# Kernel optimization log

Hardware: AMD Instinct MI355X
Metric: run time of the kernel (lower is better)

The kernel has to match this reference:

```python
import jax, jax.numpy as jnp
import numpy as np

N_NODES = 50000
N_EDGES = 800000
IN_CH = 128
OUT_CH = 64


def setup_inputs() -> dict:
    key = jax.random.key(0)
    ks = jax.random.split(key, 8)
    cat = IN_CH + OUT_CH
    scale = 1.0 / np.sqrt(cat)
    return {
        "x": jax.random.normal(ks[0], (N_NODES, IN_CH), dtype=jnp.float32),
        "edge_index": jax.random.randint(ks[1], (2, N_EDGES), 0, N_NODES, dtype=jnp.int64),
        "edge_weight": jax.random.uniform(ks[2], (N_EDGES,), dtype=jnp.float32),
        "hidden_state": jax.random.normal(ks[3], (N_NODES, OUT_CH), dtype=jnp.float32),
        "W_z": jax.random.normal(ks[4], (cat, OUT_CH), dtype=jnp.float32) * scale,
        "b_z": jnp.zeros((OUT_CH,), dtype=jnp.float32),
        "W_r": jax.random.normal(ks[5], (cat, OUT_CH), dtype=jnp.float32) * scale,
        "b_r": jnp.zeros((OUT_CH,), dtype=jnp.float32),
        "W_h": jax.random.normal(ks[6], (cat, OUT_CH), dtype=jnp.float32) * scale,
        "b_h": jnp.zeros((OUT_CH,), dtype=jnp.float32),
    }


def _gcn_norm(row, col, w, num_nodes):
    # PyG GCNConv normalization with self-loops (fill_value=1):
    # norm_e = deg[row]^-1/2 * w_e * deg[col]^-1/2 over loop-augmented edges
    loops = jnp.arange(num_nodes, dtype=row.dtype)
    row = jnp.concatenate([row, loops])
    col = jnp.concatenate([col, loops])
    w = jnp.concatenate([w, jnp.ones((num_nodes,), dtype=w.dtype)])
    deg = jax.ops.segment_sum(w, col, num_segments=num_nodes)
    dinv = jnp.where(deg > 0, jax.lax.rsqrt(deg), 0.0)
    norm = dinv[row] * w * dinv[col]
    return row, col, norm


def _gcn_conv(x_cat, W, b, row, col, norm, num_nodes):
    h = x_cat @ W                                   # (N, out)
    msg = h[row] * norm[:, None]                    # (E+N, out) gather + scale
    out = jax.ops.segment_sum(msg, col, num_segments=num_nodes)
    return out + b


def reference(x, edge_index, edge_weight, hidden_state,
              W_z, b_z, W_r, b_r, W_h, b_h):
    n = x.shape[0]
    row, col, norm = _gcn_norm(edge_index[0], edge_index[1], edge_weight, n)
    xh = jnp.concatenate([x, hidden_state], axis=1)
    z = jax.nn.sigmoid(_gcn_conv(xh, W_z, b_z, row, col, norm, n))
    r = jax.nn.sigmoid(_gcn_conv(xh, W_r, b_r, row, col, norm, n))
    xrh = jnp.concatenate([x, r * hidden_state], axis=1)
    h_cand = jnp.tanh(_gcn_conv(xrh, W_h, b_h, row, col, norm, n))
    return z * hidden_state + (1.0 - z) * h_cand
```

## Files before the change

### kernel.cpp

```cpp
#include <hip/hip_runtime.h>
#include <hip/hip_bf16.h>
#include <cstdint>
#include <cstddef>

#define IN_CH   128
#define OUT_CH  64
#define CAT_CH  192

typedef short bf16x8 __attribute__((ext_vector_type(8)));
typedef float f32x4  __attribute__((ext_vector_type(4)));
typedef float f32x2  __attribute__((ext_vector_type(2)));
typedef unsigned long long u64;
typedef unsigned int u32;

__device__ __forceinline__ float sigmoidf_(float x) { return 1.f / (1.f + __expf(-x)); }

__device__ __forceinline__ unsigned short f2bf(float f) {
    u32 u = __float_as_uint(f);
    u32 r = (u + 0x7fffu + ((u >> 16) & 1u)) >> 16;
    return (unsigned short)r;
}
__device__ __forceinline__ float bflo(u32 v) { return __uint_as_float(v << 16); }
__device__ __forceinline__ float bfhi(u32 v) { return __uint_as_float(v & 0xffff0000u); }

__device__ __forceinline__ unsigned char f2e4m3(float f) {
    u32 p = __builtin_amdgcn_cvt_pk_fp8_f32(f, f, 0, false);
    return (unsigned char)p;
}
template <bool HI>
__device__ __forceinline__ f32x2 fp8pk(u32 v) {
    return __builtin_amdgcn_cvt_pk_f32_fp8((int)v, HI);
}

__global__ void detect_kernel(const unsigned int* __restrict__ ei, int* __restrict__ flag) {
    unsigned int v = ei[(threadIdx.x << 1) + 1];
    unsigned long long b = __ballot(v != 0u);
    if (threadIdx.x == 0) *flag = (b != 0ull) ? 1 : 0;
}

__device__ __forceinline__ int load_col(const void* ei, int i, int E, int f) {
    return f ? ((const int*)ei)[E + i] : (int)((const long long*)ei)[E + i];
}
__device__ __forceinline__ int load_row(const void* ei, int i, int E, int f) {
    return f ? ((const int*)ei)[i] : (int)((const long long*)ei)[i];
}

__global__ void zero16_kernel(int4* __restrict__ p, int n16) {
    int i = blockIdx.x * blockDim.x + threadIdx.x;
    if (i < n16) p[i] = make_int4(0, 0, 0, 0);
}

__global__ void hist2_kernel(const void* __restrict__ ei, const float* __restrict__ w,
                             u64* __restrict__ packed8, u32* __restrict__ rank,
                             const int* __restrict__ flag, int E, int N) {
    int i0 = (blockIdx.x * blockDim.x + threadIdx.x) * 2;
    if (i0 >= E) return;
    const u32 shard = blockIdx.x & 7;
    u64* __restrict__ shp = packed8 + (size_t)shard * N;
    int f = *flag;
    u32 rk[2];
#pragma unroll
    for (int k = 0; k < 2; k++) {
        int i = i0 + k;
        if (i < E) {
            int c = load_col(ei, i, E, f);
            u32 wq = __float2uint_rn(w[i] * 1048576.0f);
            u64 old = atomicAdd(&shp[c], (1ull << 32) | (u64)wq);
            rk[k] = (shard << 28) | (u32)(old >> 32);
        }
    }
#pragma unroll
    for (int k = 0; k < 2; k++)
        if (i0 + k < E) rank[i0 + k] = rk[k];
}

__global__ __launch_bounds__(256) void scan1_kernel(const u64* __restrict__ packed8,
                                                    float* __restrict__ dinv,
                                                    u32* __restrict__ shoff,
                                                    int* __restrict__ starts,
                                                    int* __restrict__ bsum, int n) {
    __shared__ int s[256];
    int i = blockIdx.x * 256 + threadIdx.x;
    int v = 0;
    if (i < n) {
        u32 run = 0, wsum = 0;
#pragma unroll
        for (int sh = 0; sh < 8; sh++) {
            u64 p = packed8[(size_t)sh * n + i];
            shoff[(size_t)sh * n + i] = run;
            run  += (u32)(p >> 32);
            wsum += (u32)p;
        }
        float ws = (float)wsum * (1.0f / 1048576.0f);
        dinv[i] = rsqrtf(1.0f + ws);
        v = (int)run;
    }
    s[threadIdx.x] = v;
    __syncthreads();
#pragma unroll
    for (int d = 1; d < 256; d <<= 1) {
        int t = (threadIdx.x >= d) ? s[threadIdx.x - d] : 0;
        __syncthreads();
        s[threadIdx.x] += t;
        __syncthreads();
    }
    if (i < n) starts[i] = s[threadIdx.x] - v;
    if (threadIdx.x == 255) bsum[blockIdx.x] = s[255];
}

__global__ __launch_bounds__(256) void scan2_kernel(int* __restrict__ bsum, int nb) {
    __shared__ int s[256];
    int t = threadIdx.x;
    int v = (t < nb) ? bsum[t] : 0;
    s[t] = v;
    __syncthreads();
#pragma unroll
    for (int d = 1; d < 256; d <<= 1) {
        int u = (t >= d) ? s[t - d] : 0;
        __syncthreads();
        s[t] += u;
        __syncthreads();
    }
    if (t < nb) bsum[t] = s[t] - v;
}

__global__ void scan3_kernel(int* __restrict__ starts, const int* __restrict__ boff,
                             int n, int E) {
    int i = blockIdx.x * blockDim.x + threadIdx.x;
    if (i == 0) starts[n] = E;
    if (i < n) starts[i] += boff[blockIdx.x];
}

__global__ void scatter2_kernel(const void* __restrict__ ei, const float* __restrict__ w,
                                const float* __restrict__ dinv, const int* __restrict__ starts,
                                const u32* __restrict__ shoff, const u32* __restrict__ rank,
                                u64* __restrict__ pairs, const int* __restrict__ flag,
                                int E, int N) {
    int i0 = (blockIdx.x * blockDim.x + threadIdx.x) * 4;
    if (i0 >= E) return;
    int f = *flag;
    int r[4], c[4];
#pragma unroll
    for (int k = 0; k < 4; k++) {
        int i = i0 + k;
        if (i < E) { r[k] = load_row(ei, i, E, f); c[k] = load_col(ei, i, E, f); }
    }
#pragma unroll
    for (int k = 0; k < 4; k++) {
        int i = i0 + k;
        if (i < E) {
            float nm = dinv[r[k]] * w[i] * dinv[c[k]];
            u32 rk = rank[i];
            u32 sh = rk >> 28, rks = rk & 0x0fffffffu;
            int pos = starts[c[k]] + (int)shoff[(size_t)sh * N + c[k]] + (int)rks;
            pairs[pos] = ((u64)__float_as_uint(nm) << 32) | (u32)(r[k] << 7);
        }
    }
}

__global__ void cvt_kernel(const float* __restrict__ x, const float* __restrict__ hidden,
                           unsigned short* __restrict__ xb, unsigned short* __restrict__ hb,
                           int nx, int nh) {
    int i4 = (blockIdx.x * blockDim.x + threadIdx.x) * 4;
    if (i4 < nx) {
        float4 v = *(const float4*)&x[i4];
        ushort4 o = { f2bf(v.x), f2bf(v.y), f2bf(v.z), f2bf(v.w) };
        *(ushort4*)&xb[i4] = o;
    } else {
        int j = i4 - nx;
        if (j < nh) {
            float4 v = *(const float4*)&hidden[j];
            ushort4 o = { f2bf(v.x), f2bf(v.y), f2bf(v.z), f2bf(v.w) };
            *(ushort4*)&hb[j] = o;
        }
    }
}

__global__ void packW_kernel(const float* __restrict__ Wz, const float* __restrict__ Wr,
                             const float* __restrict__ Wh,
                             unsigned short* __restrict__ Bzrt, unsigned short* __restrict__ Wht) {
    int i = blockIdx.x * blockDim.x + threadIdx.x;
    if (i >= 192 * CAT_CH) return;
    int col = i / CAT_CH, k = i % CAT_CH;
    if (col < 128) {
        float v = (col < 64) ? Wz[k * 64 + col] : Wr[k * 64 + (col - 64)];
        Bzrt[col * CAT_CH + k] = f2bf(v);
    } else {
        Wht[(col - 128) * CAT_CH + k] = f2bf(Wh[k * 64 + (col - 128)]);
    }
}

template <int TN, bool FP8OUT>
__global__ __launch_bounds__(256) void gemm_bf16_kernel(
    const unsigned short* __restrict__ A0, int a0w,
    const unsigned short* __restrict__ A1, int a1w,
    const unsigned short* __restrict__ Bt,
    void* __restrict__ Cout, int nrows)
{
    __shared__ unsigned short As[128][48];
    __shared__ unsigned short Bs[TN][200];

    const int t = threadIdx.x, lane = t & 63, wave = t >> 6;
    const int rowBase = blockIdx.x * 128;

    for (int idx = t * 8; idx < TN * CAT_CH; idx += 256 * 8) {
        int col = idx / CAT_CH, k = idx % CAT_CH;
        *(int4*)&Bs[col][k] = *(const int4*)&Bt[idx];
    }

    f32x4 acc[2][TN / 16];
#pragma unroll
    for (int rf = 0; rf < 2; rf++)
#pragma unroll
        for (int cf = 0; cf < TN / 16; cf++) acc[rf][cf] = (f32x4){0.f, 0.f, 0.f, 0.f};

    const int srow = t >> 1, half = t & 1;
    int arow = rowBase + srow;
    if (arow >= nrows) arow = nrows - 1;

    for (int k0 = 0; k0 < CAT_CH; k0 += 32) {
        __syncthreads();
        {
            const unsigned short* src = (k0 < a0w)
                ? A0 + (size_t)arow * a0w + k0
                : A1 + (size_t)arow * a1w + (k0 - a0w);
            *(int4*)&As[srow][half * 16] = *(const int4*)(src + half * 16);
            *(int4*)&As[srow][half * 16 + 8] = *(const int4*)(src + half * 16 + 8);
        }
        __syncthreads();

        const int rbase = wave * 32;
        const int koff = (lane >> 4) * 8;
        bf16x8 a0 = *(const bf16x8*)&As[rbase + (lane & 15)][koff];
        bf16x8 a1 = *(const bf16x8*)&As[rbase + 16 + (lane & 15)][koff];
#pragma unroll
        for (int cf = 0; cf < TN / 16; cf++) {
            bf16x8 b = *(const bf16x8*)&Bs[cf * 16 + (lane & 15)][k0 + koff];
            acc[0][cf] = __builtin_amdgcn_mfma_f32_16x16x32_bf16(a0, b, acc[0][cf], 0, 0, 0);
            acc[1][cf] = __builtin_amdgcn_mfma_f32_16x16x32_bf16(a1, b, acc[1][cf], 0, 0, 0);
        }
    }

#pragma unroll
    for (int rf = 0; rf < 2; rf++)
#pragma unroll
        for (int cf = 0; cf < TN / 16; cf++) {
            int row0 = rowBase + wave * 32 + rf * 16 + (lane >> 4) * 4;
            int col  = cf * 16 + (lane & 15);
#pragma unroll
            for (int r = 0; r < 4; r++) {
                int row = row0 + r;
                if (row < nrows) {
                    if (FP8OUT)
                        ((unsigned char*)Cout)[(size_t)row * TN + col] = f2e4m3(acc[rf][cf][r]);
                    else
                        ((unsigned short*)Cout)[(size_t)row * TN + col] = f2bf(acc[rf][cf][r]);
                }
            }
        }
}

__global__ __launch_bounds__(256) void spmm_zr_kernel(
    const unsigned char* __restrict__ H8, const u64* __restrict__ pairs,
    const int* __restrict__ starts, const float* __restrict__ dinv,
    const float* __restrict__ hidden, const float* __restrict__ bz,
    const float* __restrict__ br, float* __restrict__ Z,
    unsigned short* __restrict__ RHb, int N)
{
    int node = (blockIdx.x * 256 + threadIdx.x) >> 6;
    if (node >= N) return;
    const int lane = threadIdx.x & 63;
    const int sub = lane & 31, half = lane >> 5;
    int s = starts[node], e = starts[node + 1];
    float d = dinv[node], d2 = d * d;

    float a0 = 0.f, a1 = 0.f, a2 = 0.f, a3 = 0.f;
    if (half == 0) {
        u32 sv = *(const u32*)&H8[(size_t)node * 128 + sub * 4];
        f32x2 s01 = fp8pk<false>(sv), s23 = fp8pk<true>(sv);
        a0 = s01.x * d2; a1 = s01.y * d2; a2 = s23.x * d2; a3 = s23.y * d2;
    }

    int j = s;
    int full = s + ((e - s) & ~15);
    for (; j < full; j += 16) {
        u32 hv[8]; float nm[8];
#pragma unroll
        for (int k = 0; k < 8; k++) {
            u64 p = pairs[j + k * 2 + half];
            nm[k] = __uint_as_float((u32)(p >> 32));
            hv[k] = *(const u32*)&H8[(size_t)(u32)p + sub * 4];
        }
#pragma unroll
        for (int k = 0; k < 8; k++) {
            f32x2 h01 = fp8pk<false>(hv[k]), h23 = fp8pk<true>(hv[k]);
            a0 = fmaf(h01.x, nm[k], a0); a1 = fmaf(h01.y, nm[k], a1);
            a2 = fmaf(h23.x, nm[k], a2); a3 = fmaf(h23.y, nm[k], a3);
        }
    }
    if (j < e) {
        u32 hv[8]; float nm[8];
#pragma unroll
        for (int k = 0; k < 8; k++) {
            int jj = j + k * 2 + half;
            u64 p = pairs[(jj < e) ? jj : (e - 1)];
            nm[k] = (jj < e) ? __uint_as_float((u32)(p >> 32)) : 0.f;
            hv[k] = *(const u32*)&H8[(size_t)(u32)p + sub * 4];
        }
#pragma unroll
        for (int k = 0; k < 8; k++) {
            f32x2 h01 = fp8pk<false>(hv[k]), h23 = fp8pk<true>(hv[k]);
            a0 = fmaf(h01.x, nm[k], a0); a1 = fmaf(h01.y, nm[k], a1);
            a2 = fmaf(h23.x, nm[k], a2); a3 = fmaf(h23.y, nm[k], a3);
        }
    }

    a0 += __shfl_xor(a0, 32, 64);
    a1 += __shfl_xor(a1, 32, 64);
    a2 += __shfl_xor(a2, 32, 64);
    a3 += __shfl_xor(a3, 32, 64);

    if (half == 0) {
        if (sub < 16) {
            int c = sub * 4;
            float4 b4 = *(const float4*)&bz[c];
            float4 o = { sigmoidf_(a0 + b4.x), sigmoidf_(a1 + b4.y),
                         sigmoidf_(a2 + b4.z), sigmoidf_(a3 + b4.w) };
            *(float4*)&Z[(size_t)node * 64 + c] = o;
        } else {
            int c = (sub - 16) * 4;
            float4 b4 = *(const float4*)&br[c];
            float4 hid = *(const float4*)&hidden[(size_t)node * 64 + c];
            float r0 = sigmoidf_(a0 + b4.x) * hid.x;
            float r1 = sigmoidf_(a1 + b4.y) * hid.y;
            float r2 = sigmoidf_(a2 + b4.z) * hid.z;
            float r3 = sigmoidf_(a3 + b4.w) * hid.w;
            ushort4 o = { f2bf(r0), f2bf(r1), f2bf(r2), f2bf(r3) };
            *(ushort4*)&RHb[(size_t)node * 64 + c] = o;
        }
    }
}

__global__ __launch_bounds__(256) void spmm_h_kernel(
    const unsigned short* __restrict__ H, const u64* __restrict__ pairs,
    const int* __restrict__ starts, const float* __restrict__ dinv,
    const float* __restrict__ hidden, const float* __restrict__ bh,
    const float* __restrict__ Z, float* __restrict__ out, int N)
{
    int node = (blockIdx.x * 256 + threadIdx.x) >> 6;
    if (node >= N) return;
    const int lane = threadIdx.x & 63;
    const int sub = lane & 31, half = lane >> 5;
    const unsigned char* Hb = (const unsigned char*)H;
    int s = starts[node], e = starts[node + 1];
    float d = dinv[node], d2 = d * d;

    float ax = 0.f, ay = 0.f;
    if (half == 0) {
        u32 sv = *(const u32*)&Hb[(size_t)node * 128 + sub * 4];
        ax = bflo(sv) * d2; ay = bfhi(sv) * d2;
    }

    int j = s;
    int full = s + ((e - s) & ~15);
    for (; j < full; j += 16) {
        u32 hv[8]; float nm[8];
#pragma unroll
        for (int k = 0; k < 8; k++) {
            u64 p = pairs[j + k * 2 + half];
            nm[k] = __uint_as_float((u32)(p >> 32));
            hv[k] = *(const u32*)&Hb[(size_t)(u32)p + sub * 4];
        }
#pragma unroll
        for (int k = 0; k < 8; k++) {
            ax = fmaf(bflo(hv[k]), nm[k], ax);
            ay = fmaf(bfhi(hv[k]), nm[k], ay);
        }
    }
    if (j < e) {
        u32 hv[8]; float nm[8];
#pragma unroll
        for (int k = 0; k < 8; k++) {
            int jj = j + k * 2 + half;
            u64 p = pairs[(jj < e) ? jj : (e - 1)];
            nm[k] = (jj < e) ? __uint_as_float((u32)(p >> 32)) : 0.f;
            hv[k] = *(const u32*)&Hb[(size_t)(u32)p + sub * 4];
        }
#pragma unroll
        for (int k = 0; k < 8; k++) {
            ax = fmaf(bflo(hv[k]), nm[k], ax);
            ay = fmaf(bfhi(hv[k]), nm[k], ay);
        }
    }

    ax += __shfl_xor(ax, 32, 64);
    ay += __shfl_xor(ay, 32, 64);

    if (half == 0) {
        int c = sub * 2;
        size_t idx = (size_t)node * 64 + c;
        float2 hid = *(const float2*)&hidden[idx];
        float2 z   = *(const float2*)&Z[idx];
        float hc0 = tanhf(ax + bh[c]);
        float hc1 = tanhf(ay + bh[c + 1]);
        float2 o = { z.x * hid.x + (1.f - z.x) * hc0,
                     z.y * hid.y + (1.f - z.y) * hc1 };
        *(float2*)&out[idx] = o;
    }
}

extern "C" void kernel_launch(void* const* d_in, const int* in_sizes, int n_in,
                              void* d_out, int out_size, void* d_ws, size_t ws_size,
                              hipStream_t stream) {
    const float* x      = (const float*)d_in[0];
    const void*  eidx   = d_in[1];
    const float* ew     = (const float*)d_in[2];
    const float* hidden = (const float*)d_in[3];
    const float* Wz     = (const float*)d_in[4];
    const float* bz     = (const float*)d_in[5];
    const float* Wr     = (const float*)d_in[6];
    const float* br     = (const float*)d_in[7];
    const float* Wh     = (const float*)d_in[8];
    const float* bh     = (const float*)d_in[9];
    float* out = (float*)d_out;

    const int E = in_sizes[2];
    const int N = in_sizes[3] / OUT_CH;

    char* base = (char*)d_ws;
    size_t off = 0;
    auto carve = [&](size_t bytes) -> char* {
        char* p = base + off;
        off = (off + bytes + 255) & ~(size_t)255;
        return p;
    };
    u64*   packed8 = (u64*) carve((size_t)N * 8 * 8);
    u32*   shoff   = (u32*) carve((size_t)N * 8 * 4);
    u32*   rank    = (u32*) carve((size_t)E * 4);
    float* dinv    = (float*)carve((size_t)N * 4);
    int*   starts  = (int*)  carve((size_t)(N + 1) * 4);
    int*   bsum    = (int*)  carve(256 * 4);
    u64*   pairs   = (u64*)  carve((size_t)E * 8);
    unsigned short* xb   = (unsigned short*)carve((size_t)N * 128 * 2);
    unsigned short* hb   = (unsigned short*)carve((size_t)N * 64 * 2);
    unsigned char*  Hzr8 = (unsigned char*)carve((size_t)N * 128);
    unsigned short* RHb  = (unsigned short*)carve((size_t)N * 64 * 2);
    unsigned short* Hhb  = (unsigned short*)carve((size_t)N * 64 * 2);
    float* Z = (float*)carve((size_t)N * 64 * 4);
    unsigned short* Bzrt = (unsigned short*)carve((size_t)128 * CAT_CH * 2);
    unsigned short* Wht  = (unsigned short*)carve((size_t)64 * CAT_CH * 2);
    int* flag = (int*)carve(4);
    if (off > ws_size) return;

    const int B256 = 256;
    const int gE2 = (E + 511) / 512;
    const int gE4 = (E + 1023) / 1024;
    const int gN = (N + B256 - 1) / B256;
    const int gM = (N + 127) / 128;
    const int gW = (N + 3) / 4;
    const int n16 = N * 4;
    const int gZ = (n16 + B256 - 1) / B256;

    hipLaunchKernelGGL(detect_kernel, dim3(1), dim3(64), 0, stream,
                       (const unsigned int*)eidx, flag);

    hipLaunchKernelGGL(zero16_kernel, dim3(gZ), dim3(B256), 0, stream,
                       (int4*)packed8, n16);
    hipLaunchKernelGGL(hist2_kernel, dim3(gE2), dim3(B256), 0, stream,
                       eidx, ew, packed8, rank, flag, E, N);

    hipLaunchKernelGGL(scan1_kernel, dim3(gN), dim3(B256), 0, stream,
                       packed8, dinv, shoff, starts, bsum, N);
    hipLaunchKernelGGL(scan2_kernel, dim3(1), dim3(B256), 0, stream, bsum, gN);
    hipLaunchKernelGGL(scan3_kernel, dim3(gN), dim3(B256), 0, stream, starts, bsum, N, E);

    hipLaunchKernelGGL(scatter2_kernel, dim3(gE4), dim3(B256), 0, stream,
                       eidx, ew, dinv, starts, shoff, rank, pairs, flag, E, N);

    hipLaunchKernelGGL(cvt_kernel, dim3((N * CAT_CH / 4 + 255) / 256), dim3(B256), 0, stream,
                       x, hidden, xb, hb, N * 128, N * 64);
    hipLaunchKernelGGL(packW_kernel, dim3((192 * CAT_CH + 255) / 256), dim3(B256), 0, stream,
                       Wz, Wr, Wh, Bzrt, Wht);

    hipLaunchKernelGGL((gemm_bf16_kernel<128, true>), dim3(gM), dim3(B256), 0, stream,
                       xb, 128, hb, 64, Bzrt, (void*)Hzr8, N);

    hipLaunchKernelGGL(spmm_zr_kernel, dim3(gW), dim3(B256), 0, stream,
                       Hzr8, pairs, starts, dinv, hidden, bz, br, Z, RHb, N);

    hipLaunchKernelGGL((gemm_bf16_kernel<64, false>), dim3(gM), dim3(B256), 0, stream,
                       xb, 128, RHb, 64, Wht, (void*)Hhb, N);

    hipLaunchKernelGGL(spmm_h_kernel, dim3(gW), dim3(B256), 0, stream,
                       Hhb, pairs, starts, dinv, hidden, bh, Z, out, N);
}
```

Baseline: 180.3 us.

## Split GEMM outputs into 64-byte column planes and gather each plane separately

The GEMM now writes its output as two planar halves (z vs r for the fp8 output, two 32-column halves for the bf16 output), each with a 64-byte row stride. Edge pair offsets are rescaled from row<<7 to row<<6 to match. The SpMM kernels launch twice as many blocks, one set per plane, and use 16 lanes per edge with 4 edges in flight per wave. The goal is a smaller gathered working set per pass, so it fits better in cache and has higher locality. In exchange, the pair list and index metadata are read twice, and there are extra shuffle reductions.

```diff
diff --git a/kernel.cpp b/kernel.cpp
--- a/kernel.cpp
+++ b/kernel.cpp
@@ -153,7 +153,7 @@
             u32 rk = rank[i];
             u32 sh = rk >> 28, rks = rk & 0x0fffffffu;
             int pos = starts[c[k]] + (int)shoff[(size_t)sh * N + c[k]] + (int)rks;
-            pairs[pos] = ((u64)__float_as_uint(nm) << 32) | (u32)(r[k] << 7);
+            pairs[pos] = ((u64)__float_as_uint(nm) << 32) | (u32)(r[k] << 6);
         }
     }
 }
@@ -251,10 +251,13 @@
             for (int r = 0; r < 4; r++) {
                 int row = row0 + r;
                 if (row < nrows) {
-                    if (FP8OUT)
-                        ((unsigned char*)Cout)[(size_t)row * TN + col] = f2e4m3(acc[rf][cf][r]);
-                    else
-                        ((unsigned short*)Cout)[(size_t)row * TN + col] = f2bf(acc[rf][cf][r]);
+                    if (FP8OUT) {
+                        size_t idx = ((size_t)(col >> 6) * nrows + row) * 64 + (col & 63);
+                        ((unsigned char*)Cout)[idx] = f2e4m3(acc[rf][cf][r]);
+                    } else {
+                        size_t idx = ((size_t)(col >> 5) * nrows + row) * 32 + (col & 31);
+                        ((unsigned short*)Cout)[idx] = f2bf(acc[rf][cf][r]);
+                    }
                 }
             }
         }
@@ -265,18 +268,21 @@
     const int* __restrict__ starts, const float* __restrict__ dinv,
     const float* __restrict__ hidden, const float* __restrict__ bz,
     const float* __restrict__ br, float* __restrict__ Z,
-    unsigned short* __restrict__ RHb, int N)
+    unsigned short* __restrict__ RHb, int N, int nodeBlocks)
 {
-    int node = (blockIdx.x * 256 + threadIdx.x) >> 6;
+    const int plane = (blockIdx.x >= nodeBlocks) ? 1 : 0;
+    const int nb = blockIdx.x - plane * nodeBlocks;
+    int node = nb * 4 + (threadIdx.x >> 6);
     if (node >= N) return;
     const int lane = threadIdx.x & 63;
-    const int sub = lane & 31, half = lane >> 5;
+    const int sub = lane & 15, q = lane >> 4;
+    const unsigned char* __restrict__ Hp = H8 + (size_t)plane * N * 64;
     int s = starts[node], e = starts[node + 1];
     float d = dinv[node], d2 = d * d;
 
     float a0 = 0.f, a1 = 0.f, a2 = 0.f, a3 = 0.f;
-    if (half == 0) {
-        u32 sv = *(const u32*)&H8[(size_t)node * 128 + sub * 4];
+    if (q == 0) {
+        u32 sv = *(const u32*)&Hp[(size_t)node * 64 + sub * 4];
         f32x2 s01 = fp8pk<false>(sv), s23 = fp8pk<true>(sv);
         a0 = s01.x * d2; a1 = s01.y * d2; a2 = s23.x * d2; a3 = s23.y * d2;
     }
@@ -284,51 +290,50 @@
     int j = s;
     int full = s + ((e - s) & ~15);
     for (; j < full; j += 16) {
-        u32 hv[8]; float nm[8];
-#pragma unroll
-        for (int k = 0; k < 8; k++) {
-            u64 p = pairs[j + k * 2 + half];
+        u32 hv[4]; float nm[4];
+#pragma unroll
+        for (int k = 0; k < 4; k++) {
+            u64 p = pairs[j + k * 4 + q];
             nm[k] = __uint_as_float((u32)(p >> 32));
-            hv[k] = *(const u32*)&H8[(size_t)(u32)p + sub * 4];
-        }
-#pragma unroll
-        for (int k = 0; k < 8; k++) {
+            hv[k] = *(const u32*)&Hp[(size_t)(u32)p + sub * 4];
+        }
+#pragma unroll
+        for (int k = 0; k < 4; k++) {
             f32x2 h01 = fp8pk<false>(hv[k]), h23 = fp8pk<true>(hv[k]);
             a0 = fmaf(h01.x, nm[k], a0); a1 = fmaf(h01.y, nm[k], a1);
             a2 = fmaf(h23.x, nm[k], a2); a3 = fmaf(h23.y, nm[k], a3);
         }
     }
     if (j < e) {
-        u32 hv[8]; float nm[8];
-#pragma unroll
-        for (int k = 0; k < 8; k++) {
-            int jj = j + k * 2 + half;
+        u32 hv[4]; float nm[4];
+#pragma unroll
+        for (int k = 0; k < 4; k++) {
+            int jj = j + k * 4 + q;
             u64 p = pairs[(jj < e) ? jj : (e - 1)];
             nm[k] = (jj < e) ? __uint_as_float((u32)(p >> 32)) : 0.f;
-            hv[k] = *(const u32*)&H8[(size_t)(u32)p + sub * 4];
-        }
-#pragma unroll
-        for (int k = 0; k < 8; k++) {
+            hv[k] = *(const u32*)&Hp[(size_t)(u32)p + sub * 4];
+        }
+#pragma unroll
+        for (int k = 0; k < 4; k++) {
             f32x2 h01 = fp8pk<false>(hv[k]), h23 = fp8pk<true>(hv[k]);
             a0 = fmaf(h01.x, nm[k], a0); a1 = fmaf(h01.y, nm[k], a1);
             a2 = fmaf(h23.x, nm[k], a2); a3 = fmaf(h23.y, nm[k], a3);
         }
     }
 
-    a0 += __shfl_xor(a0, 32, 64);
-    a1 += __shfl_xor(a1, 32, 64);
-    a2 += __shfl_xor(a2, 32, 64);
-    a3 += __shfl_xor(a3, 32, 64);
-
-    if (half == 0) {
-        if (sub < 16) {
-            int c = sub * 4;
+    a0 += __shfl_xor(a0, 16, 64); a0 += __shfl_xor(a0, 32, 64);
+    a1 += __shfl_xor(a1, 16, 64); a1 += __shfl_xor(a1, 32, 64);
+    a2 += __shfl_xor(a2, 16, 64); a2 += __shfl_xor(a2, 32, 64);
+    a3 += __shfl_xor(a3, 16, 64); a3 += __shfl_xor(a3, 32, 64);
+
+    if (q == 0) {
+        int c = sub * 4;
+        if (plane == 0) {
             float4 b4 = *(const float4*)&bz[c];
             float4 o = { sigmoidf_(a0 + b4.x), sigmoidf_(a1 + b4.y),
                          sigmoidf_(a2 + b4.z), sigmoidf_(a3 + b4.w) };
             *(float4*)&Z[(size_t)node * 64 + c] = o;
         } else {
-            int c = (sub - 16) * 4;
             float4 b4 = *(const float4*)&br[c];
             float4 hid = *(const float4*)&hidden[(size_t)node * 64 + c];
             float r0 = sigmoidf_(a0 + b4.x) * hid.x;
@@ -345,59 +350,62 @@
     const unsigned short* __restrict__ H, const u64* __restrict__ pairs,
     const int* __restrict__ starts, const float* __restrict__ dinv,
     const float* __restrict__ hidden, const float* __restrict__ bh,
-    const float* __restrict__ Z, float* __restrict__ out, int N)
+    const float* __restrict__ Z, float* __restrict__ out, int N, int nodeBlocks)
 {
-    int node = (blockIdx.x * 256 + threadIdx.x) >> 6;
+    const int plane = (blockIdx.x >= nodeBlocks) ? 1 : 0;
+    const int nb = blockIdx.x - plane * nodeBlocks;
+    int node = nb * 4 + (threadIdx.x >> 6);
     if (node >= N) return;
     const int lane = threadIdx.x & 63;
-    const int sub = lane & 31, half = lane >> 5;
-    const unsigned char* Hb = (const unsigned char*)H;
+    const int sub = lane & 15, q = lane >> 4;
+    const unsigned char* __restrict__ Hp =
+        (const unsigned char*)H + (size_t)plane * N * 64;
     int s = starts[node], e = starts[node + 1];
     float d = dinv[node], d2 = d * d;
 
     float ax = 0.f, ay = 0.f;
-    if (half == 0) {
-        u32 sv = *(const u32*)&Hb[(size_t)node * 128 + sub * 4];
+    if (q == 0) {
+        u32 sv = *(const u32*)&Hp[(size_t)node * 64 + sub * 4];
         ax = bflo(sv) * d2; ay = bfhi(sv) * d2;
     }
 
     int j = s;
     int full = s + ((e - s) & ~15);
     for (; j < full; j += 16) {
-        u32 hv[8]; float nm[8];
-#pragma unroll
-        for (int k = 0; k < 8; k++) {
-            u64 p = pairs[j + k * 2 + half];
+        u32 hv[4]; float nm[4];
+#pragma unroll
+        for (int k = 0; k < 4; k++) {
+            u64 p = pairs[j + k * 4 + q];
             nm[k] = __uint_as_float((u32)(p >> 32));
-            hv[k] = *(const u32*)&Hb[(size_t)(u32)p + sub * 4];
-        }
-#pragma unroll
-        for (int k = 0; k < 8; k++) {
+            hv[k] = *(const u32*)&Hp[(size_t)(u32)p + sub * 4];
+        }
+#pragma unroll
+        for (int k = 0; k < 4; k++) {
             ax = fmaf(bflo(hv[k]), nm[k], ax);
             ay = fmaf(bfhi(hv[k]), nm[k], ay);
         }
     }
     if (j < e) {
-        u32 hv[8]; float nm[8];
-#pragma unroll
-        for (int k = 0; k < 8; k++) {
-            int jj = j + k * 2 + half;
+        u32 hv[4]; float nm[4];
+#pragma unroll
+        for (int k = 0; k < 4; k++) {
+            int jj = j + k * 4 + q;
             u64 p = pairs[(jj < e) ? jj : (e - 1)];
             nm[k] = (jj < e) ? __uint_as_float((u32)(p >> 32)) : 0.f;
-            hv[k] = *(const u32*)&Hb[(size_t)(u32)p + sub * 4];
-        }
-#pragma unroll
-        for (int k = 0; k < 8; k++) {
+            hv[k] = *(const u32*)&Hp[(size_t)(u32)p + sub * 4];
+        }
+#pragma unroll
+        for (int k = 0; k < 4; k++) {
             ax = fmaf(bflo(hv[k]), nm[k], ax);
             ay = fmaf(bfhi(hv[k]), nm[k], ay);
         }
     }
 
-    ax += __shfl_xor(ax, 32, 64);
-    ay += __shfl_xor(ay, 32, 64);
-
-    if (half == 0) {
-        int c = sub * 2;
+    ax += __shfl_xor(ax, 16, 64); ax += __shfl_xor(ax, 32, 64);
+    ay += __shfl_xor(ay, 16, 64); ay += __shfl_xor(ay, 32, 64);
+
+    if (q == 0) {
+        int c = plane * 32 + sub * 2;
         size_t idx = (size_t)node * 64 + c;
         float2 hid = *(const float2*)&hidden[idx];
         float2 z   = *(const float2*)&Z[idx];
@@ -485,12 +493,12 @@
     hipLaunchKernelGGL((gemm_bf16_kernel<128, true>), dim3(gM), dim3(B256), 0, stream,
                        xb, 128, hb, 64, Bzrt, (void*)Hzr8, N);
 
-    hipLaunchKernelGGL(spmm_zr_kernel, dim3(gW), dim3(B256), 0, stream,
-                       Hzr8, pairs, starts, dinv, hidden, bz, br, Z, RHb, N);
+    hipLaunchKernelGGL(spmm_zr_kernel, dim3(gW * 2), dim3(B256), 0, stream,
+                       Hzr8, pairs, starts, dinv, hidden, bz, br, Z, RHb, N, gW);
 
     hipLaunchKernelGGL((gemm_bf16_kernel<64, false>), dim3(gM), dim3(B256), 0, stream,
                        xb, 128, RHb, 64, Wht, (void*)Hhb, N);
 
-    hipLaunchKernelGGL(spmm_h_kernel, dim3(gW), dim3(B256), 0, stream,
-                       Hhb, pairs, starts, dinv, hidden, bh, Z, out, N);
-}
+    hipLaunchKernelGGL(spmm_h_kernel, dim3(gW * 2), dim3(B256), 0, stream,
+                       Hhb, pairs, starts, dinv, hidden, bh, Z, out, N, gW);
+}
```

Measured after the change: 200.9 us. +11.4%, slower.
